# Kernel tuning notes

Measured on AMD Instinct MI355X. Metric: run time of the kernel, lower is better.

Reference implementation:

```python
import jax, jax.numpy as jnp
import numpy as np

B, S, D, K = 8, 1024, 1024, 8192


def setup_inputs() -> dict:
    key = jax.random.key(0)
    k1, k2 = jax.random.split(key)
    z = jax.random.normal(k1, (B, S, D), dtype=jnp.float32)
    codebook = jax.random.normal(k2, (K, D), dtype=jnp.float32)
    return {"z": z, "codebook": codebook}


def reference(z, codebook):
    # Eval-mode forward of VectorQuantizer (no EMA / dead-code side effects).
    b, s, d = z.shape
    z_flat = z.reshape(-1, d)                              # [N, D]
    # squared L2 distances: ||z||^2 + ||e||^2 - 2 z.e
    distances = (jnp.sum(z_flat * z_flat, axis=1, keepdims=True)
                 + jnp.sum(codebook * codebook, axis=1)
                 - 2.0 * jnp.einsum('nd,kd->nk', z_flat, codebook))  # [N, K]
    indices = jnp.argmin(distances, axis=1)                # [N]
    quantized = codebook[indices].reshape(b, s, d)         # gather
    loss = jnp.asarray(0.0, dtype=z.dtype)                 # eval mode
    # straight-through estimator
    quantized = z + jax.lax.stop_gradient(quantized - z)
    logits = -distances.reshape(b, s, -1)                  # [B, S, K]
    return quantized, indices.reshape(b, s), loss, logits
```

## Files before the change

kernel.cpp:

```cpp
#include <hip/hip_runtime.h>
#include <hip/hip_bf16.h>
#include <stdint.h>

#define NROWS 8192
#define KCODES 8192
#define DDIM 1024

#define Q_OFF    0
#define IDX_OFF  8388608
#define LOSS_OFF 8396800
#define LOG_OFF  8396801

using f32x4  = __attribute__((ext_vector_type(4))) float;
using i32x4  = __attribute__((ext_vector_type(4))) int;

__device__ __forceinline__ unsigned int forder(float f) {
  unsigned int u = __float_as_uint(f);
  return (u & 0x80000000u) ? ~u : (u | 0x80000000u);
}
__device__ __forceinline__ float finv(unsigned int u) {
  return (u & 0x80000000u) ? __uint_as_float(u & 0x7fffffffu) : __uint_as_float(~u);
}

__device__ __forceinline__ void gld_lds16(const void* g, void* l) {
  __builtin_amdgcn_global_load_lds((const __attribute__((address_space(1))) unsigned int*)g,
                                   (__attribute__((address_space(3))) unsigned int*)l,
                                   16, 0, 0);
}

__global__ __launch_bounds__(256) void vq_convert(const float* __restrict__ z,
                                                  const float* __restrict__ cb,
                                                  signed char* __restrict__ qbuf,
                                                  float* __restrict__ nrm,
                                                  float* __restrict__ scl,
                                                  unsigned int* __restrict__ gmins) {
  const int r = blockIdx.x;
  const int tid = threadIdx.x;
  if (r < 1024) gmins[r * 256 + tid] = 0xFFFFFFFFu;

  const float* src = (r < NROWS) ? (z + (size_t)r * DDIM)
                                 : (cb + (size_t)(r - NROWS) * DDIM);
  float4 v = reinterpret_cast<const float4*>(src)[tid];
  float vv[4] = {v.x, v.y, v.z, v.w};

  float amax = fmaxf(fmaxf(fabsf(vv[0]), fabsf(vv[1])),
                     fmaxf(fabsf(vv[2]), fabsf(vv[3])));
  float ss = vv[0]*vv[0] + vv[1]*vv[1] + vv[2]*vv[2] + vv[3]*vv[3];
  #pragma unroll
  for (int m = 32; m > 0; m >>= 1) {
    amax = fmaxf(amax, __shfl_down(amax, m, 64));
    ss += __shfl_down(ss, m, 64);
  }
  __shared__ float rA[4], rS[4], sB;
  if ((tid & 63) == 0) { rA[tid >> 6] = amax; rS[tid >> 6] = ss; }
  __syncthreads();
  if (tid == 0) {
    const float a = fmaxf(fmaxf(rA[0], rA[1]), fmaxf(rA[2], rA[3]));
    nrm[r] = rS[0] + rS[1] + rS[2] + rS[3];
    const float s = fmaxf(a, 1e-20f) * (1.0f / 127.0f);
    scl[r] = s;
    sB = s;
  }
  __syncthreads();
  const float inv = 1.0f / sB;
  int q[4];
  #pragma unroll
  for (int j = 0; j < 4; ++j) {
    int t = (int)rintf(vv[j] * inv);
    q[j] = t < -127 ? -127 : (t > 127 ? 127 : t);
  }
  const int packed = (q[0] & 255) | ((q[1] & 255) << 8) |
                     ((q[2] & 255) << 16) | (q[3] << 24);
  reinterpret_cast<int*>(qbuf + (size_t)r * DDIM)[tid] = packed;
}

__global__ __launch_bounds__(256, 4) void vq_mfma(const signed char* __restrict__ zq,
                                                  const signed char* __restrict__ cq,
                                                  const float* __restrict__ nrm,
                                                  const float* __restrict__ scl,
                                                  unsigned int* __restrict__ gmins,
                                                  float* __restrict__ out) {
  __shared__ i32x4 lds[2048];

  const int wgid = blockIdx.x;
  const int stx = wgid & 7;
  const int idx = wgid >> 3;
  const int sty = idx >> 6;
  const int tt_ = idx & 63;
  const int bx = stx * 8 + (tt_ & 7);
  const int by = sty * 8 + (tt_ >> 3);

  const int k0 = bx * 128;
  const int n0 = by * 128;
  const int tid = threadIdx.x;
  const int wid = tid >> 6, lane = tid & 63;
  const int wm = wid >> 1, wn = wid & 1;
  const int l15 = lane & 15, l4 = lane >> 4;

  const signed char* ga[2];
  const signed char* gb[2];
  int ldst[2];
  #pragma unroll
  for (int q = 0; q < 2; ++q) {
    const int s = wid * 2 + q;
    const int row = s * 16 + (lane >> 2);
    const int cg = (lane & 3) ^ ((row >> 1) & 3);
    ga[q] = zq + (size_t)(n0 + row) * DDIM + cg * 16;
    gb[q] = cq + (size_t)(k0 + row) * DDIM + cg * 16;
    ldst[q] = s * 1024;
  }

  auto stage = [&](int t, int b) {
    const int d0 = t * 64;
    #pragma unroll
    for (int q = 0; q < 2; ++q)
      gld_lds16(ga[q] + d0, (char*)lds + b * 16384 + ldst[q]);
    #pragma unroll
    for (int q = 0; q < 2; ++q)
      gld_lds16(gb[q] + d0, (char*)lds + b * 16384 + 8192 + ldst[q]);
  };

  i32x4 acc[4][4];
  #pragma unroll
  for (int i = 0; i < 4; ++i)
    #pragma unroll
    for (int j = 0; j < 4; ++j) acc[i][j] = (i32x4){0, 0, 0, 0};

  stage(0, 0);
  asm volatile("s_waitcnt vmcnt(0)" ::: "memory");
  __builtin_amdgcn_s_barrier();

  #pragma unroll 2
  for (int t = 0; t < 16; ++t) {
    const int cur = t & 1;
    if (t < 15) stage(t + 1, cur ^ 1);
    const int base = cur * 1024;
    i32x4 af[4], bf[4];
    #pragma unroll
    for (int f = 0; f < 4; ++f) {
      const int ar = wm * 64 + f * 16 + l15;
      af[f] = lds[base + ar * 4 + (l4 ^ ((ar >> 1) & 3))];
      const int br = wn * 64 + f * 16 + l15;
      bf[f] = lds[base + 512 + br * 4 + (l4 ^ ((br >> 1) & 3))];
    }
    asm volatile("s_waitcnt lgkmcnt(0)" ::: "memory");
    __builtin_amdgcn_sched_barrier(0);
    __builtin_amdgcn_s_setprio(1);
    #pragma unroll
    for (int fm = 0; fm < 4; ++fm)
      #pragma unroll
      for (int fn = 0; fn < 4; ++fn)
        acc[fm][fn] = __builtin_amdgcn_mfma_i32_16x16x64_i8(af[fm], bf[fn], acc[fm][fn], 0, 0, 0);
    __builtin_amdgcn_s_setprio(0);
    if (t < 15) {
      asm volatile("s_waitcnt vmcnt(0)" ::: "memory");
      __builtin_amdgcn_s_barrier();
    }
  }

  float ee[4], sk[4];
  #pragma unroll
  for (int j = 0; j < 4; ++j) {
    const int kk = k0 + wn * 64 + j * 16 + l15;
    ee[j] = nrm[NROWS + kk];
    sk[j] = scl[NROWS + kk];
  }

  float* logits = out + LOG_OFF;
  #pragma unroll
  for (int f = 0; f < 4; ++f) {
    #pragma unroll
    for (int r = 0; r < 4; ++r) {
      const int n = n0 + wm * 64 + f * 16 + l4 * 4 + r;
      const float zz = nrm[n];
      const float sn2 = -2.0f * scl[n];
      float rowmin = 3.4e38f;
      #pragma unroll
      for (int j = 0; j < 4; ++j) {
        const int k = k0 + wn * 64 + j * 16 + l15;
        const float dist = fmaf(sn2 * sk[j], (float)acc[f][j][r], zz + ee[j]);
        logits[(size_t)n * KCODES + k] = -dist;
        rowmin = fminf(rowmin, dist);
      }
      #pragma unroll
      for (int mm = 1; mm < 16; mm <<= 1)
        rowmin = fminf(rowmin, __shfl_xor(rowmin, mm, 64));
      if (l15 == 0) atomicMin(&gmins[(size_t)n * 32 + (bx >> 1)], forder(rowmin));
    }
  }
}

#define MARGIN 16.0f
__global__ __launch_bounds__(256) void vq_refine(const float* __restrict__ z,
                                                 const float* __restrict__ cb,
                                                 const float* __restrict__ nrm,
                                                 const unsigned int* __restrict__ gmins,
                                                 float* __restrict__ out) {
  const int n = blockIdx.x;
  const int tid = threadIdx.x;
  __shared__ float tminS[32];
  __shared__ float gminS;
  __shared__ int cnt;
  __shared__ int cand[64];
  __shared__ float red[4];

  if (tid < 32) tminS[tid] = finv(gmins[(size_t)n * 32 + tid]);
  if (tid == 0) cnt = 0;
  __syncthreads();
  if (tid == 0) {
    float g = tminS[0];
    #pragma unroll
    for (int i = 1; i < 32; ++i) g = fminf(g, tminS[i]);
    gminS = g;
  }
  __syncthreads();
  const float thr = gminS + MARGIN;

  const float* lrow = out + LOG_OFF + (size_t)n * KCODES;
  for (int g = 0; g < 32; ++g) {
    if (tminS[g] <= thr) {
      const float dist = -lrow[g * 256 + tid];
      if (dist <= thr) {
        const int p = atomicAdd(&cnt, 1);
        if (p < 64) cand[p] = g * 256 + tid;
      }
    }
  }
  __syncthreads();
  const int ncand = min(cnt, 64);

  const float zz = nrm[n];
  const float4 zv = reinterpret_cast<const float4*>(z + (size_t)n * DDIM)[tid];
  float bestd = 0.f;
  int bestk = -1;
  for (int ci = 0; ci < ncand; ++ci) {
    const int k = cand[ci];
    const float4 ev = reinterpret_cast<const float4*>(cb + (size_t)k * DDIM)[tid];
    float s = zv.x * ev.x + zv.y * ev.y + zv.z * ev.z + zv.w * ev.w;
    #pragma unroll
    for (int mm = 32; mm > 0; mm >>= 1) s += __shfl_down(s, mm, 64);
    if ((tid & 63) == 0) red[tid >> 6] = s;
    __syncthreads();
    const float dot = red[0] + red[1] + red[2] + red[3];
    const float dist = zz + nrm[NROWS + k] - 2.0f * dot;
    if (bestk < 0 || dist < bestd || (dist == bestd && k < bestk)) {
      bestd = dist; bestk = k;
    }
    __syncthreads();
  }

  const float4* src = reinterpret_cast<const float4*>(cb + (size_t)bestk * DDIM);
  float4* dst = reinterpret_cast<float4*>(out + (size_t)n * DDIM);
  dst[tid] = src[tid];
  if (tid == 0) {
    out[IDX_OFF + n] = (float)bestk;
    if (n == 0) out[LOSS_OFF] = 0.f;
  }
}

extern "C" void kernel_launch(void* const* d_in, const int* in_sizes, int n_in,
                              void* d_out, int out_size, void* d_ws, size_t ws_size,
                              hipStream_t stream) {
  const float* z  = (const float*)d_in[0];
  const float* cb = (const float*)d_in[1];
  float* out = (float*)d_out;

  float* nrm = (float*)d_ws;
  float* scl = (float*)((char*)d_ws + 65536);
  unsigned int* gmins = (unsigned int*)((char*)d_ws + 131072);

  signed char* qbuf = (signed char*)out;
  const signed char* zq = qbuf;
  const signed char* cq = qbuf + (size_t)NROWS * DDIM;

  vq_convert<<<NROWS + KCODES, 256, 0, stream>>>(z, cb, qbuf, nrm, scl, gmins);
  vq_mfma<<<4096, 256, 0, stream>>>(zq, cq, nrm, scl, gmins, out);
  vq_refine<<<NROWS, 256, 0, stream>>>(z, cb, nrm, gmins, out);
}
```

Measured before the change: 202.1 us.

## Stage logits tile through LDS for aligned vectorized 16-byte global stores

The logits region starts at float offset LOG_OFF = 8396801, so it is not 16-byte aligned and each lane used to write scalar, scattered floats. The tile's logits are now written into a swizzled LDS buffer in two halves. Threads then copy them out as aligned float4 stores, shifted by three columns to match the alignment. The three leading and one trailing columns per row are still written as scalars. This aims to coalesce the large logits write stream, at the cost of extra LDS traffic, barriers and recomputed distances.

```diff
diff --git a/kernel.cpp b/kernel.cpp
--- a/kernel.cpp
+++ b/kernel.cpp
@@ -177,15 +177,57 @@
       float rowmin = 3.4e38f;
       #pragma unroll
       for (int j = 0; j < 4; ++j) {
-        const int k = k0 + wn * 64 + j * 16 + l15;
+        const int col = wn * 64 + j * 16 + l15;
         const float dist = fmaf(sn2 * sk[j], (float)acc[f][j][r], zz + ee[j]);
-        logits[(size_t)n * KCODES + k] = -dist;
+        if ((j == 0 && wn == 0 && l15 < 3) || (j == 3 && wn == 1 && l15 == 15))
+          logits[(size_t)n * KCODES + k0 + col] = -dist;
         rowmin = fminf(rowmin, dist);
       }
       #pragma unroll
       for (int mm = 1; mm < 16; mm <<= 1)
         rowmin = fminf(rowmin, __shfl_xor(rowmin, mm, 64));
       if (l15 == 0) atomicMin(&gmins[(size_t)n * 32 + (bx >> 1)], forder(rowmin));
+    }
+  }
+
+  float* tb = (float*)lds;
+  const int rr = tid >> 5;
+  const int cc = tid & 31;
+  #pragma unroll 1
+  for (int p = 0; p < 2; ++p) {
+    __syncthreads();
+    if (wm == p) {
+      #pragma unroll
+      for (int f = 0; f < 4; ++f) {
+        #pragma unroll
+        for (int r = 0; r < 4; ++r) {
+          const int rowl = f * 16 + l4 * 4 + r;
+          const int n = n0 + p * 64 + rowl;
+          const float zz = nrm[n];
+          const float sn2 = -2.0f * scl[n];
+          const int swz = (rowl & 7) << 2;
+          #pragma unroll
+          for (int j = 0; j < 4; ++j) {
+            const int col = wn * 64 + j * 16 + l15;
+            if (col >= 3 && col <= 126) {
+              const float dist = fmaf(sn2 * sk[j], (float)acc[f][j][r], zz + ee[j]);
+              const int cl = col - 3;
+              tb[rowl * 128 + (((cl & ~3) ^ swz)) + (cl & 3)] = -dist;
+            }
+          }
+        }
+      }
+    }
+    __syncthreads();
+    if (cc < 31) {
+      #pragma unroll
+      for (int it = 0; it < 8; ++it) {
+        const int rowl = it * 8 + rr;
+        const f32x4 v = *reinterpret_cast<const f32x4*>(
+            tb + rowl * 128 + ((4 * cc) ^ ((rowl & 7) << 2)));
+        *reinterpret_cast<f32x4*>(
+            out + LOG_OFF + (size_t)(n0 + p * 64 + rowl) * KCODES + k0 + 3 + 4 * cc) = v;
+      }
     }
   }
 }
```

Result: slower. 335.5 us (+66.0%).
